# Optimization experiments

Hardware: AMD Instinct MI355X
Metric: run time of the kernel (lower is better)

The kernel has to match this reference:

```python
import jax, jax.numpy as jnp
import numpy as np

N, E, D, H, C, ED = 30000, 300000, 256, 8, 32, 32
HID = H * C  # 256 = hidden_channels


def setup_inputs() -> dict:
    key = jax.random.key(0)
    ks = jax.random.split(key, 14)
    w = lambda k, shp, fan: (jax.random.normal(k, shp, jnp.float32) / np.sqrt(fan)).astype(jnp.float32)
    return {
        "x": jax.random.normal(ks[0], (N, D), jnp.float32),
        "edge_index": jax.random.randint(ks[1], (2, E), 0, N, jnp.int32),
        "edge_attr": jax.random.normal(ks[2], (E, ED), jnp.float32),
        # TransformerConv params (PyG: q/k/v Linears have bias; lin_edge & lin_skip bias=False)
        "Wq": w(ks[3], (D, HID), D), "bq": 0.01 * jax.random.normal(ks[4], (HID,), jnp.float32),
        "Wk": w(ks[5], (D, HID), D), "bk": 0.01 * jax.random.normal(ks[6], (HID,), jnp.float32),
        "Wv": w(ks[7], (D, HID), D), "bv": 0.01 * jax.random.normal(ks[8], (HID,), jnp.float32),
        "We": w(ks[9], (ED, HID), ED),
        "Wskip": w(ks[10], (D, HID), D),
        # MLP([HID, HID, HID], gelu-tanh, plain_last=False): two Linear+act layers
        "W1": w(ks[11], (HID, HID), HID), "b1": jnp.zeros((HID,), jnp.float32),
        "W2": w(ks[12], (HID, HID), HID), "b2": jnp.zeros((HID,), jnp.float32),
    }


def reference(x, edge_index, edge_attr, Wq, bq, Wk, bk, Wv, bv, We, Wskip, W1, b1, W2, b2):
    src, dst = edge_index[0], edge_index[1]  # message flows src -> dst
    q = (x @ Wq + bq).reshape(N, H, C)
    k = (x @ Wk + bk).reshape(N, H, C)
    v = (x @ Wv + bv).reshape(N, H, C)
    e = (edge_attr @ We).reshape(E, H, C)
    k_e = k[src] + e                               # [E,H,C]
    v_e = v[src] + e                               # [E,H,C]
    logits = jnp.einsum('ehc,ehc->eh', q[dst], k_e) / np.sqrt(C)  # [E,H]
    # segment softmax over incoming edges of each dst node
    m = jax.ops.segment_max(logits, dst, num_segments=N)          # [N,H]
    a = jnp.exp(logits - m[dst])
    denom = jax.ops.segment_sum(a, dst, num_segments=N)           # [N,H]
    alpha = a / (denom[dst] + 1e-16)                              # [E,H]
    agg = jax.ops.segment_sum(alpha[:, :, None] * v_e, dst, num_segments=N)  # [N,H,C]
    out = agg.reshape(N, HID) + x @ Wskip          # concat heads + root skip
    # residual MLP: x + gelu(gelu(x W1 + b1) W2 + b2)
    h = jax.nn.gelu(out @ W1 + b1, approximate=True)
    h = jax.nn.gelu(h @ W2 + b2, approximate=True)
    return out + h
```

## Files before the change

kernel.cpp:

```cpp
#include <hip/hip_runtime.h>

#define NN 30000
#define NE 300000
#define HIDDEN 256

typedef __attribute__((ext_vector_type(8))) __bf16 bf16x8;
typedef __attribute__((ext_vector_type(4))) __bf16 bf16x4;
typedef __attribute__((ext_vector_type(4))) float float4v;

__device__ inline __bf16 f2bf(float f) {
  unsigned u = __builtin_bit_cast(unsigned, f);
  u += 0x7fffu + ((u >> 16) & 1u);
  unsigned short s = (unsigned short)(u >> 16);
  return __builtin_bit_cast(__bf16, s);
}
__device__ inline float bf2f(__bf16 b) {
  unsigned short s = __builtin_bit_cast(unsigned short, b);
  unsigned u = ((unsigned)s) << 16;
  return __builtin_bit_cast(float, u);
}
__device__ inline float gelu_tanh(float x) {
  float x3 = x * x * x;
  return 0.5f * x * (1.0f + tanhf(0.79788456080286536f * (x + 0.044715f * x3)));
}

#define PREP_XB_END (1829 + (NN * 32 + 255) / 256)
__global__ __launch_bounds__(256) void prep_kernel(
    const float* __restrict__ Wq, const float* __restrict__ Wk, const float* __restrict__ Wv,
    const float* __restrict__ Wsk, const float* __restrict__ W1, const float* __restrict__ W2,
    const float* __restrict__ We, const float* __restrict__ bq, const float* __restrict__ bk,
    const float* __restrict__ bv, const float* __restrict__ x,
    __bf16* __restrict__ WTall, __bf16* __restrict__ WT1, __bf16* __restrict__ WT2,
    float* __restrict__ ball, float* __restrict__ WeT, __bf16* __restrict__ xb,
    int* __restrict__ degz) {
  const int b = blockIdx.x;
  const int tid = threadIdx.x;
  if (b < 1792) {
    const int region = b >> 8;
    const int idx = ((b & 255) << 8) | tid;
    const int k = idx & 255, n = idx >> 8;
    float v;
    if (region == 3) {
      const int h = n >> 5, d = n & 31;
      const float* wq = Wq + (size_t)k * 256 + h * 32;
      const float* we = We + (size_t)d * 256 + h * 32;
      float s = 0.f;
#pragma unroll
      for (int c = 0; c < 32; ++c) s += wq[c] * we[c];
      v = s;
    } else {
      const float* W = (region == 0) ? Wq : (region == 1) ? Wk : (region == 2) ? Wv
                     : (region == 4) ? Wsk : (region == 5) ? W1 : W2;
      v = W[(size_t)k * 256 + n];
    }
    const __bf16 bv16 = f2bf(v);
    if (region < 5) WTall[(size_t)region * 65536 + idx] = bv16;
    else if (region == 5) WT1[idx] = bv16;
    else WT2[idx] = bv16;
  } else if (b < 1797) {
    const int j = (b - 1792) * 256 + tid;
    if (j < 1280) {
      float v = 0.f;
      if (j < 256) v = bq[j];
      else if (j < 512) v = bk[j - 256];
      else if (j < 768) v = bv[j - 512];
      else if (j < 1024) {
        const int col = j - 768, h = col >> 5, d = col & 31;
        const float* bqh = bq + h * 32;
        const float* we = We + (size_t)d * 256 + h * 32;
        float s = 0.f;
#pragma unroll
        for (int c = 0; c < 32; ++c) s += bqh[c] * we[c];
        v = s;
      }
      ball[j] = v;
    }
  } else if (b < 1829) {
    const int idx = (b - 1797) * 256 + tid;
    const int ch = idx >> 5, d = idx & 31;
    WeT[idx] = We[(size_t)d * 256 + ch];
  } else if (b < PREP_XB_END) {
    const int t = (b - 1829) * 256 + tid;
    if (t < NN * 256 / 8) {
      const float* p = x + (size_t)t * 8;
      float4v f0 = *(const float4v*)(p);
      float4v f1 = *(const float4v*)(p + 4);
      bf16x8 o;
#pragma unroll
      for (int j = 0; j < 4; ++j) { o[j] = f2bf(f0[j]); o[j + 4] = f2bf(f1[j]); }
      *(bf16x8*)(xb + (size_t)t * 8) = o;
    }
  } else {
    const int idx = (b - PREP_XB_END) * 256 + tid;
    if (idx < 2 * NN) degz[idx] = 0;
  }
}

__global__ void count_deg_kernel(const int* __restrict__ dst, int* __restrict__ deg, int E) {
  int e = blockIdx.x * 256 + threadIdx.x;
  if (e < E) atomicAdd(&deg[dst[e]], 1);
}

__global__ __launch_bounds__(256) void deg_psum_kernel(const int* __restrict__ deg,
                                                       int* __restrict__ psum, int n) {
  int i = blockIdx.x * 256 + threadIdx.x;
  int v = (i < n) ? deg[i] : 0;
#pragma unroll
  for (int s = 1; s < 64; s <<= 1) v += __shfl_xor(v, s);
  __shared__ int ws[4];
  if ((threadIdx.x & 63) == 0) ws[threadIdx.x >> 6] = v;
  __syncthreads();
  if (threadIdx.x == 0) psum[blockIdx.x] = ws[0] + ws[1] + ws[2] + ws[3];
}

__global__ __launch_bounds__(128) void psum_scan_kernel(int* __restrict__ psum,
                                                        int* __restrict__ offs, int nb) {
  __shared__ int tmp[128];
  const int t = threadIdx.x;
  int v = (t < nb) ? psum[t] : 0;
  tmp[t] = v;
  __syncthreads();
  for (int s = 1; s < 128; s <<= 1) {
    int u = (t >= s) ? tmp[t - s] : 0;
    __syncthreads();
    tmp[t] += u;
    __syncthreads();
  }
  if (t < nb) psum[t] = tmp[t] - v;
  if (t == 0) offs[NN] = NE;
}

__global__ __launch_bounds__(256) void offs_kernel(const int* __restrict__ deg,
                                                   const int* __restrict__ psum,
                                                   int* __restrict__ offs, int n) {
  __shared__ int tmp[256];
  const int t = threadIdx.x;
  const int i = blockIdx.x * 256 + t;
  int v = (i < n) ? deg[i] : 0;
  tmp[t] = v;
  __syncthreads();
  for (int s = 1; s < 256; s <<= 1) {
    int u = (t >= s) ? tmp[t - s] : 0;
    __syncthreads();
    tmp[t] += u;
    __syncthreads();
  }
  if (i < n) offs[i] = psum[blockIdx.x] + tmp[t] - v;
}

__global__ void scatter_kernel(const int* __restrict__ srcIn, const int* __restrict__ dstIn,
                               const int* __restrict__ offs, int* __restrict__ cursor,
                               int2* __restrict__ sed, int E) {
  int e = blockIdx.x * 256 + threadIdx.x;
  if (e >= E) return;
  int d = dstIn[e];
  int p = atomicAdd(&cursor[d], 1);
  sed[offs[d] + p] = make_int2(srcIn[e], e);
}

template <int GX, int EPI, int MODE>
__global__ __launch_bounds__(256) void gemm_k4(
    const __bf16* __restrict__ A, const __bf16* __restrict__ Wt,
    const float* __restrict__ bias,
    float* __restrict__ Yf, __bf16* __restrict__ Ybf,
    __bf16* __restrict__ QGp, __bf16* __restrict__ KVp,
    const float* __restrict__ resid, int M, int gyTiles) {
  __shared__ char smem[128 * 264 * 2];
  __bf16* Bs = (__bf16*)smem;
  const int bid = blockIdx.x;
  const int stripe = bid / (8 * GX);
  const int rem = bid % (8 * GX);
  const int y8 = rem % 8;
  const int xt = rem / 8;
  const int y = stripe * 8 + y8;
  if (y >= gyTiles) return;
  const int n0 = xt * 128;

  {
    const int t = threadIdx.x;
#pragma unroll
    for (int i = 0; i < 16; ++i) {
      int g = i * 256 + t;
      int row = g >> 5;
      int c16 = g & 31;
      bf16x8 v = *(const bf16x8*)(Wt + (size_t)(n0 + row) * 256 + c16 * 8);
      *(bf16x8*)(Bs + row * 264 + c16 * 8) = v;
    }
  }
  __syncthreads();

  const int lane = threadIdx.x & 63;
  const int w = threadIdx.x >> 6;
  const int r = lane & 15;
  const int q = lane >> 4;
  const int mw = y * 128 + w * 32;
  int ar0 = mw + r;      if (ar0 >= M) ar0 = M - 1;
  int ar1 = mw + 16 + r; if (ar1 >= M) ar1 = M - 1;
  const int kq = q * 8;

  float4v acc[2][8];
#pragma unroll
  for (int i = 0; i < 2; ++i)
#pragma unroll
    for (int t = 0; t < 8; ++t) acc[i][t] = (float4v){0.f, 0.f, 0.f, 0.f};

#pragma unroll
  for (int kk = 0; kk < 256; kk += 32) {
    const int ka = kk + kq;
    bf16x8 a0 = *(const bf16x8*)(A + (size_t)ar0 * 256 + ka);
    bf16x8 a1 = *(const bf16x8*)(A + (size_t)ar1 * 256 + ka);
    bf16x8 b[8];
#pragma unroll
    for (int t = 0; t < 8; ++t)
      b[t] = *(const bf16x8*)(Bs + (t * 16 + r) * 264 + ka);
#pragma unroll
    for (int t = 0; t < 8; ++t) {
      acc[0][t] = __builtin_amdgcn_mfma_f32_16x16x32_bf16(a0, b[t], acc[0][t], 0, 0, 0);
      acc[1][t] = __builtin_amdgcn_mfma_f32_16x16x32_bf16(a1, b[t], acc[1][t], 0, 0, 0);
    }
  }
  __syncthreads();

  float* cs = (float*)smem + w * 4224;
#pragma unroll
  for (int t = 0; t < 8; ++t) {
    const int col = n0 + t * 16 + r;
    const float bb = bias ? bias[col] : 0.0f;
#pragma unroll
    for (int i2 = 0; i2 < 2; ++i2)
#pragma unroll
      for (int ii = 0; ii < 4; ++ii) {
        float v = acc[i2][t][ii] + bb;
        if constexpr (EPI == 2 || EPI == 3) v = gelu_tanh(v);
        cs[(i2 * 16 + q * 4 + ii) * 132 + t * 16 + r] = v;
      }
  }

  constexpr int NSTR = GX * 128;
  const int p = n0 >> 8;
  const int cbase = n0 & 255;
  __bf16* dstI = (p == 0 || p == 3) ? QGp : KVp;
  const int moff = (p >= 2) ? 4 : 0;
#pragma unroll
  for (int i = 0; i < 16; ++i) {
    const int rl = i * 2 + (lane >> 5);
    const int row = mw + rl;
    const int c4 = (lane & 31) * 4;
    float4v v = *(const float4v*)(cs + rl * 132 + c4);
    if (row < M) {
      if constexpr (MODE == 1) {
        if (p == 4) {
          *(float4v*)(Yf + (size_t)row * 256 + cbase + c4) = v;
        } else {
          bf16x4 b4;
          b4[0] = f2bf(v[0]); b4[1] = f2bf(v[1]); b4[2] = f2bf(v[2]); b4[3] = f2bf(v[3]);
          const int c = cbase + c4;
          *(bf16x4*)(dstI + (size_t)row * 512 + 2 * c + moff) = b4;
        }
      } else if constexpr (EPI == 1) {
        *(float4v*)(Yf + (size_t)row * NSTR + n0 + c4) = v;
      } else if constexpr (EPI == 3) {
        float4v rr = *(const float4v*)(resid + (size_t)row * NSTR + n0 + c4);
        v[0] += rr[0]; v[1] += rr[1]; v[2] += rr[2]; v[3] += rr[3];
        *(float4v*)(Yf + (size_t)row * NSTR + n0 + c4) = v;
      } else {
        bf16x4 b4;
        b4[0] = f2bf(v[0]); b4[1] = f2bf(v[1]); b4[2] = f2bf(v[2]); b4[3] = f2bf(v[3]);
        *(bf16x4*)(Ybf + (size_t)row * NSTR + n0 + c4) = b4;
      }
    }
  }
}

__global__ __launch_bounds__(256) void attn_kernel(
    const __bf16* __restrict__ QG, const __bf16* __restrict__ KV,
    const float* __restrict__ ea, const int2* __restrict__ sed,
    const int* __restrict__ offs,
    float* __restrict__ OUT, __bf16* __restrict__ AE) {
  __shared__ float sdn[4][64];
  __shared__ float sav[4][64][4], sae[4][64][4];
  const int lane = threadIdx.x & 63;
  const int w = threadIdx.x >> 6;
  const int n = blockIdx.x;
  const int sub = lane & 7;

  const float LSC = 0.25506589858f;
  const bf16x8 qg = *(const bf16x8*)(QG + (size_t)n * 512 + lane * 8);
  const float q0 = bf2f(qg[0]) * LSC, q1 = bf2f(qg[1]) * LSC;
  const float q2 = bf2f(qg[2]) * LSC, q3 = bf2f(qg[3]) * LSC;
  const float g0 = bf2f(qg[4]) * LSC, g1 = bf2f(qg[5]) * LSC;
  const float g2 = bf2f(qg[6]) * LSC, g3 = bf2f(qg[7]) * LSC;

  float denom = 0.f;
  float4v accv = {0.f, 0.f, 0.f, 0.f};
  float4v acce = {0.f, 0.f, 0.f, 0.f};
  const int beg = offs[n], end = offs[n + 1];

  int i = beg + w;
  for (; i + 4 < end; i += 8) {
    const int2 s0 = sed[i];
    const int2 s1 = sed[i + 4];
    const bf16x8 kv0 = *(const bf16x8*)(KV + (size_t)s0.x * 512 + lane * 8);
    const float4v e0 = *(const float4v*)(ea + (size_t)s0.y * 32 + sub * 4);
    const bf16x8 kv1 = *(const bf16x8*)(KV + (size_t)s1.x * 512 + lane * 8);
    const float4v e1 = *(const float4v*)(ea + (size_t)s1.y * 32 + sub * 4);
    float p0 = q0 * bf2f(kv0[0]) + q1 * bf2f(kv0[1]) + q2 * bf2f(kv0[2]) + q3 * bf2f(kv0[3])
             + g0 * e0[0] + g1 * e0[1] + g2 * e0[2] + g3 * e0[3];
    float p1 = q0 * bf2f(kv1[0]) + q1 * bf2f(kv1[1]) + q2 * bf2f(kv1[2]) + q3 * bf2f(kv1[3])
             + g0 * e1[0] + g1 * e1[1] + g2 * e1[2] + g3 * e1[3];
    p0 += __shfl_xor(p0, 1); p1 += __shfl_xor(p1, 1);
    p0 += __shfl_xor(p0, 2); p1 += __shfl_xor(p1, 2);
    p0 += __shfl_xor(p0, 4); p1 += __shfl_xor(p1, 4);
    const float w0 = exp2f(p0);
    const float w1 = exp2f(p1);
    denom += w0 + w1;
    accv[0] += w0 * bf2f(kv0[4]) + w1 * bf2f(kv1[4]);
    accv[1] += w0 * bf2f(kv0[5]) + w1 * bf2f(kv1[5]);
    accv[2] += w0 * bf2f(kv0[6]) + w1 * bf2f(kv1[6]);
    accv[3] += w0 * bf2f(kv0[7]) + w1 * bf2f(kv1[7]);
    acce[0] += w0 * e0[0] + w1 * e1[0];
    acce[1] += w0 * e0[1] + w1 * e1[1];
    acce[2] += w0 * e0[2] + w1 * e1[2];
    acce[3] += w0 * e0[3] + w1 * e1[3];
  }
  if (i < end) {
    const int2 s0 = sed[i];
    const bf16x8 kv0 = *(const bf16x8*)(KV + (size_t)s0.x * 512 + lane * 8);
    const float4v e0 = *(const float4v*)(ea + (size_t)s0.y * 32 + sub * 4);
    float p0 = q0 * bf2f(kv0[0]) + q1 * bf2f(kv0[1]) + q2 * bf2f(kv0[2]) + q3 * bf2f(kv0[3])
             + g0 * e0[0] + g1 * e0[1] + g2 * e0[2] + g3 * e0[3];
    p0 += __shfl_xor(p0, 1);
    p0 += __shfl_xor(p0, 2);
    p0 += __shfl_xor(p0, 4);
    const float w0 = exp2f(p0);
    denom += w0;
    accv[0] += w0 * bf2f(kv0[4]);
    accv[1] += w0 * bf2f(kv0[5]);
    accv[2] += w0 * bf2f(kv0[6]);
    accv[3] += w0 * bf2f(kv0[7]);
    acce[0] += w0 * e0[0];
    acce[1] += w0 * e0[1];
    acce[2] += w0 * e0[2];
    acce[3] += w0 * e0[3];
  }

  sdn[w][lane] = denom;
#pragma unroll
  for (int j = 0; j < 4; ++j) { sav[w][lane][j] = accv[j]; sae[w][lane][j] = acce[j]; }
  __syncthreads();
  if (w == 0) {
    float D = 0.f;
    float4v av = {0.f, 0.f, 0.f, 0.f};
    float4v ae = {0.f, 0.f, 0.f, 0.f};
#pragma unroll
    for (int ww = 0; ww < 4; ++ww) {
      D += sdn[ww][lane];
#pragma unroll
      for (int j = 0; j < 4; ++j) { av[j] += sav[ww][lane][j]; ae[j] += sae[ww][lane][j]; }
    }
    const float inv = 1.0f / (D + 1e-16f);
    const int c0 = lane * 4;
    float4v o = *(const float4v*)(OUT + (size_t)n * 256 + c0);
#pragma unroll
    for (int j = 0; j < 4; ++j) o[j] += av[j] * inv;
    *(float4v*)(OUT + (size_t)n * 256 + c0) = o;
    bf16x4 aeb;
    aeb[0] = f2bf(ae[0] * inv); aeb[1] = f2bf(ae[1] * inv);
    aeb[2] = f2bf(ae[2] * inv); aeb[3] = f2bf(ae[3] * inv);
    *(bf16x4*)(AE + (size_t)n * 256 + c0) = aeb;
  }
}

__global__ __launch_bounds__(256) void post_kernel(
    const __bf16* __restrict__ AE, const float* __restrict__ WeT,
    float* __restrict__ OUT, __bf16* __restrict__ OUTh) {
  const int lane = threadIdx.x & 63;
  const int wave = threadIdx.x >> 6;
  const int c0 = lane * 4;
  const int hg = lane >> 3;

  float4v w4[4][8];
#pragma unroll
  for (int j = 0; j < 4; ++j)
#pragma unroll
    for (int s = 0; s < 8; ++s)
      w4[j][s] = *(const float4v*)(WeT + (size_t)(c0 + j) * 32 + s * 4);

  const int nbase = blockIdx.x * 64;
  for (int it = 0; it < 16; ++it) {
    const int n = nbase + it * 4 + wave;
    if (n >= NN) return;
    const __bf16* aerow = AE + (size_t)n * HIDDEN + hg * 32;
    float aef[32];
#pragma unroll
    for (int t = 0; t < 4; ++t) {
      bf16x8 a8 = *(const bf16x8*)(aerow + t * 8);
#pragma unroll
      for (int j = 0; j < 8; ++j) aef[t * 8 + j] = bf2f(a8[j]);
    }
    float4v o = *(const float4v*)(OUT + (size_t)n * HIDDEN + c0);
#pragma unroll
    for (int j = 0; j < 4; ++j) {
      float s = 0.f;
#pragma unroll
      for (int g = 0; g < 8; ++g) {
        s += aef[g * 4 + 0] * w4[j][g][0] + aef[g * 4 + 1] * w4[j][g][1]
           + aef[g * 4 + 2] * w4[j][g][2] + aef[g * 4 + 3] * w4[j][g][3];
      }
      o[j] += s;
    }
    *(float4v*)(OUT + (size_t)n * HIDDEN + c0) = o;
    bf16x4 ob;
    ob[0] = f2bf(o[0]); ob[1] = f2bf(o[1]); ob[2] = f2bf(o[2]); ob[3] = f2bf(o[3]);
    *(bf16x4*)(OUTh + (size_t)n * HIDDEN + c0) = ob;
  }
}

extern "C" void kernel_launch(void* const* d_in, const int* in_sizes, int n_in,
                              void* d_out, int out_size, void* d_ws, size_t ws_size,
                              hipStream_t stream) {
  (void)in_sizes; (void)n_in; (void)out_size; (void)ws_size;
  const float* x   = (const float*)d_in[0];
  const int*   ei  = (const int*)d_in[1];
  const float* ea  = (const float*)d_in[2];
  const float* Wq  = (const float*)d_in[3];
  const float* bq  = (const float*)d_in[4];
  const float* Wk  = (const float*)d_in[5];
  const float* bk  = (const float*)d_in[6];
  const float* Wv  = (const float*)d_in[7];
  const float* bv  = (const float*)d_in[8];
  const float* We  = (const float*)d_in[9];
  const float* Wsk = (const float*)d_in[10];
  const float* W1  = (const float*)d_in[11];
  const float* b1  = (const float*)d_in[12];
  const float* W2  = (const float*)d_in[13];
  const float* b2  = (const float*)d_in[14];
  float* out = (float*)d_out;

  char* ws = (char*)d_ws;
  size_t off = 0;
  auto alloc = [&](size_t bytes) -> char* {
    off = (off + 255) & ~(size_t)255;
    char* p = ws + off;
    off += bytes;
    return p;
  };
  __bf16* QG   = (__bf16*)alloc((size_t)NN * 512 * 2);
  __bf16* KV   = (__bf16*)alloc((size_t)NN * 512 * 2);
  __bf16* xb   = (__bf16*)alloc((size_t)NN * 256 * 2);
  __bf16* AE   = (__bf16*)alloc((size_t)NN * 256 * 2);
  __bf16* OUTh = (__bf16*)alloc((size_t)NN * 256 * 2);
  __bf16* WTall = (__bf16*)alloc((size_t)1280 * 256 * 2);
  __bf16* WT1  = (__bf16*)alloc(256 * 256 * 2);
  __bf16* WT2  = (__bf16*)alloc(256 * 256 * 2);
  float*  ball = (float*)alloc(1280 * 4);
  float*  WeT  = (float*)alloc(256 * 32 * 4);
  int* deg    = (int*)alloc((size_t)2 * NN * 4);
  int* cursor = deg + NN;
  int* offs   = (int*)alloc((size_t)(NN + 1) * 4);
  int* psum   = (int*)alloc(512);
  int2* sed   = (int2*)alloc((size_t)NE * 8);
  __bf16* H1 = AE;

  const int* srcIn = ei;
  const int* dstIn = ei + NE;

  const int prepBlocks = PREP_XB_END + (2 * NN + 255) / 256;
  prep_kernel<<<prepBlocks, 256, 0, stream>>>(Wq, Wk, Wv, Wsk, W1, W2, We, bq, bk, bv, x,
                                              WTall, WT1, WT2, ball, WeT, xb, deg);

  const int nb = (NN + 255) / 256;
  count_deg_kernel<<<(NE + 255) / 256, 256, 0, stream>>>(dstIn, deg, NE);
  deg_psum_kernel<<<nb, 256, 0, stream>>>(deg, psum, NN);
  psum_scan_kernel<<<1, 128, 0, stream>>>(psum, offs, nb);
  offs_kernel<<<nb, 256, 0, stream>>>(deg, psum, offs, NN);
  scatter_kernel<<<(NE + 255) / 256, 256, 0, stream>>>(srcIn, dstIn, offs, cursor, sed, NE);

  const int gy = (NN + 127) / 128;
  const int stripes = (gy + 7) / 8;
  gemm_k4<10, 0, 1><<<stripes * 80, 256, 0, stream>>>(
      xb, WTall, ball, out, nullptr, QG, KV, nullptr, NN, gy);

  attn_kernel<<<NN, 256, 0, stream>>>(QG, KV, ea, sed, offs, out, AE);

  post_kernel<<<(NN + 63) / 64, 256, 0, stream>>>(AE, WeT, out, OUTh);

  gemm_k4<2, 2, 0><<<stripes * 16, 256, 0, stream>>>(
      OUTh, WT1, b1, nullptr, H1, nullptr, nullptr, nullptr, NN, gy);
  gemm_k4<2, 3, 0><<<stripes * 16, 256, 0, stream>>>(
      H1, WT2, b2, out, nullptr, nullptr, nullptr, out, NN, gy);
}
```

Before: 371.2 us.

## Permute edge attributes into dst-sorted bf16 layout during scatter

The scatter kernel now reads each edge's 32 float attributes, converts them to bf16, and writes them into a CSR-ordered buffer at the edge's sorted position. It stores only the source index instead of a (src, edge id) pair. The attention kernel then reads edge attributes contiguously by sorted position at half the bytes, rather than gathering fp32 rows by original edge id. In exchange the scatter pass does an extra full read and write of the edge features, and the edge attributes lose precision by being rounded to bf16.

```diff
diff --git a/kernel.cpp b/kernel.cpp
--- a/kernel.cpp
+++ b/kernel.cpp
@@ -149,13 +149,27 @@
 }
 
 __global__ void scatter_kernel(const int* __restrict__ srcIn, const int* __restrict__ dstIn,
+                               const float* __restrict__ ea,
                                const int* __restrict__ offs, int* __restrict__ cursor,
-                               int2* __restrict__ sed, int E) {
+                               int* __restrict__ srcs, __bf16* __restrict__ eaC, int E) {
   int e = blockIdx.x * 256 + threadIdx.x;
   if (e >= E) return;
+  const float* src = ea + (size_t)e * 32;
+  float4v f[8];
+#pragma unroll
+  for (int t = 0; t < 8; ++t) f[t] = *(const float4v*)(src + t * 4);
   int d = dstIn[e];
   int p = atomicAdd(&cursor[d], 1);
-  sed[offs[d] + p] = make_int2(srcIn[e], e);
+  int o = offs[d] + p;
+  srcs[o] = srcIn[e];
+  __bf16* dstp = eaC + (size_t)o * 32;
+#pragma unroll
+  for (int t = 0; t < 4; ++t) {
+    bf16x8 b;
+#pragma unroll
+    for (int j = 0; j < 4; ++j) { b[j] = f2bf(f[t * 2][j]); b[j + 4] = f2bf(f[t * 2 + 1][j]); }
+    *(bf16x8*)(dstp + t * 8) = b;
+  }
 }
 
 template <int GX, int EPI, int MODE>
@@ -274,8 +288,8 @@
 
 __global__ __launch_bounds__(256) void attn_kernel(
     const __bf16* __restrict__ QG, const __bf16* __restrict__ KV,
-    const float* __restrict__ ea, const int2* __restrict__ sed,
-    const int* __restrict__ offs,
+    const __bf16* __restrict__ eaC,
+    const int* __restrict__ srcs, const int* __restrict__ offs,
     float* __restrict__ OUT, __bf16* __restrict__ AE) {
   __shared__ float sdn[4][64];
   __shared__ float sav[4][64][4], sae[4][64][4];
@@ -298,16 +312,18 @@
 
   int i = beg + w;
   for (; i + 4 < end; i += 8) {
-    const int2 s0 = sed[i];
-    const int2 s1 = sed[i + 4];
-    const bf16x8 kv0 = *(const bf16x8*)(KV + (size_t)s0.x * 512 + lane * 8);
-    const float4v e0 = *(const float4v*)(ea + (size_t)s0.y * 32 + sub * 4);
-    const bf16x8 kv1 = *(const bf16x8*)(KV + (size_t)s1.x * 512 + lane * 8);
-    const float4v e1 = *(const float4v*)(ea + (size_t)s1.y * 32 + sub * 4);
+    const int s0 = srcs[i];
+    const int s1 = srcs[i + 4];
+    const bf16x8 kv0 = *(const bf16x8*)(KV + (size_t)s0 * 512 + lane * 8);
+    const bf16x4 a0 = *(const bf16x4*)(eaC + (size_t)i * 32 + sub * 4);
+    const bf16x8 kv1 = *(const bf16x8*)(KV + (size_t)s1 * 512 + lane * 8);
+    const bf16x4 a1 = *(const bf16x4*)(eaC + (size_t)(i + 4) * 32 + sub * 4);
+    const float e00 = bf2f(a0[0]), e01 = bf2f(a0[1]), e02 = bf2f(a0[2]), e03 = bf2f(a0[3]);
+    const float e10 = bf2f(a1[0]), e11 = bf2f(a1[1]), e12 = bf2f(a1[2]), e13 = bf2f(a1[3]);
     float p0 = q0 * bf2f(kv0[0]) + q1 * bf2f(kv0[1]) + q2 * bf2f(kv0[2]) + q3 * bf2f(kv0[3])
-             + g0 * e0[0] + g1 * e0[1] + g2 * e0[2] + g3 * e0[3];
+             + g0 * e00 + g1 * e01 + g2 * e02 + g3 * e03;
     float p1 = q0 * bf2f(kv1[0]) + q1 * bf2f(kv1[1]) + q2 * bf2f(kv1[2]) + q3 * bf2f(kv1[3])
-             + g0 * e1[0] + g1 * e1[1] + g2 * e1[2] + g3 * e1[3];
+             + g0 * e10 + g1 * e11 + g2 * e12 + g3 * e13;
     p0 += __shfl_xor(p0, 1); p1 += __shfl_xor(p1, 1);
     p0 += __shfl_xor(p0, 2); p1 += __shfl_xor(p1, 2);
     p0 += __shfl_xor(p0, 4); p1 += __shfl_xor(p1, 4);
@@ -318,17 +334,18 @@
     accv[1] += w0 * bf2f(kv0[5]) + w1 * bf2f(kv1[5]);
     accv[2] += w0 * bf2f(kv0[6]) + w1 * bf2f(kv1[6]);
     accv[3] += w0 * bf2f(kv0[7]) + w1 * bf2f(kv1[7]);
-    acce[0] += w0 * e0[0] + w1 * e1[0];
-    acce[1] += w0 * e0[1] + w1 * e1[1];
-    acce[2] += w0 * e0[2] + w1 * e1[2];
-    acce[3] += w0 * e0[3] + w1 * e1[3];
+    acce[0] += w0 * e00 + w1 * e10;
+    acce[1] += w0 * e01 + w1 * e11;
+    acce[2] += w0 * e02 + w1 * e12;
+    acce[3] += w0 * e03 + w1 * e13;
   }
   if (i < end) {
-    const int2 s0 = sed[i];
-    const bf16x8 kv0 = *(const bf16x8*)(KV + (size_t)s0.x * 512 + lane * 8);
-    const float4v e0 = *(const float4v*)(ea + (size_t)s0.y * 32 + sub * 4);
+    const int s0 = srcs[i];
+    const bf16x8 kv0 = *(const bf16x8*)(KV + (size_t)s0 * 512 + lane * 8);
+    const bf16x4 a0 = *(const bf16x4*)(eaC + (size_t)i * 32 + sub * 4);
+    const float e00 = bf2f(a0[0]), e01 = bf2f(a0[1]), e02 = bf2f(a0[2]), e03 = bf2f(a0[3]);
     float p0 = q0 * bf2f(kv0[0]) + q1 * bf2f(kv0[1]) + q2 * bf2f(kv0[2]) + q3 * bf2f(kv0[3])
-             + g0 * e0[0] + g1 * e0[1] + g2 * e0[2] + g3 * e0[3];
+             + g0 * e00 + g1 * e01 + g2 * e02 + g3 * e03;
     p0 += __shfl_xor(p0, 1);
     p0 += __shfl_xor(p0, 2);
     p0 += __shfl_xor(p0, 4);
@@ -338,10 +355,10 @@
     accv[1] += w0 * bf2f(kv0[5]);
     accv[2] += w0 * bf2f(kv0[6]);
     accv[3] += w0 * bf2f(kv0[7]);
-    acce[0] += w0 * e0[0];
-    acce[1] += w0 * e0[1];
-    acce[2] += w0 * e0[2];
-    acce[3] += w0 * e0[3];
+    acce[0] += w0 * e00;
+    acce[1] += w0 * e01;
+    acce[2] += w0 * e02;
+    acce[3] += w0 * e03;
   }
 
   sdn[w][lane] = denom;
@@ -450,6 +467,7 @@
   __bf16* xb   = (__bf16*)alloc((size_t)NN * 256 * 2);
   __bf16* AE   = (__bf16*)alloc((size_t)NN * 256 * 2);
   __bf16* OUTh = (__bf16*)alloc((size_t)NN * 256 * 2);
+  __bf16* eaC  = (__bf16*)alloc((size_t)NE * 32 * 2);
   __bf16* WTall = (__bf16*)alloc((size_t)1280 * 256 * 2);
   __bf16* WT1  = (__bf16*)alloc(256 * 256 * 2);
   __bf16* WT2  = (__bf16*)alloc(256 * 256 * 2);
@@ -459,7 +477,7 @@
   int* cursor = deg + NN;
   int* offs   = (int*)alloc((size_t)(NN + 1) * 4);
   int* psum   = (int*)alloc(512);
-  int2* sed   = (int2*)alloc((size_t)NE * 8);
+  int* srcs   = (int*)alloc((size_t)NE * 4);
   __bf16* H1 = AE;
 
   const int* srcIn = ei;
@@ -474,14 +492,15 @@
   deg_psum_kernel<<<nb, 256, 0, stream>>>(deg, psum, NN);
   psum_scan_kernel<<<1, 128, 0, stream>>>(psum, offs, nb);
   offs_kernel<<<nb, 256, 0, stream>>>(deg, psum, offs, NN);
-  scatter_kernel<<<(NE + 255) / 256, 256, 0, stream>>>(srcIn, dstIn, offs, cursor, sed, NE);
+  scatter_kernel<<<(NE + 255) / 256, 256, 0, stream>>>(srcIn, dstIn, ea, offs, cursor,
+                                                       srcs, eaC, NE);
 
   const int gy = (NN + 127) / 128;
   const int stripes = (gy + 7) / 8;
   gemm_k4<10, 0, 1><<<stripes * 80, 256, 0, stream>>>(
       xb, WTall, ball, out, nullptr, QG, KV, nullptr, NN, gy);
 
-  attn_kernel<<<NN, 256, 0, stream>>>(QG, KV, ea, sed, offs, out, AE);
+  attn_kernel<<<NN, 256, 0, stream>>>(QG, KV, eaC, srcs, offs, out, AE);
 
   post_kernel<<<(NN + 63) / 64, 256, 0, stream>>>(AE, WeT, out, OUTh);
 
```

Result: faster. 354.7 us (-4.4%).
